# Optimization experiments

Measured on AMD Instinct MI355X. Metric: run time of the kernel, lower is better.

Reference implementation:

```python
import jax, jax.numpy as jnp
import numpy as np

# Multi-scale feature pyramid (static: determines per-level slice bounds)
SPATIAL_SHAPES = np.array([[100, 100], [50, 50], [25, 25], [13, 13], [7, 7]])  # (H, W) per level
LEVEL_START = np.concatenate([[0], np.cumsum(SPATIAL_SHAPES[:, 0] * SPATIAL_SHAPES[:, 1])])[:-1]
C = 256       # hidden_inplanes
HEADS = 8     # head_nums
POINTS = 4    # point_nums
LEVELS = 5    # feature_level_nums
FF = 2048     # feedforward_planes
DH = C // HEADS


def setup_inputs() -> dict:
    key = jax.random.key(0)
    ks = jax.random.split(key, 16)
    B = 2
    L = int((SPATIAL_SHAPES[:, 0] * SPATIAL_SHAPES[:, 1]).sum())  # 13343 tokens
    s = 0.02
    return {
        'src': jax.random.normal(ks[0], (B, L, C), jnp.float32),
        'pos': jax.random.normal(ks[1], (B, L, C), jnp.float32) * 0.1,
        'reference_points': jax.random.uniform(ks[2], (B, L, LEVELS, 2), jnp.float32),
        'wv': jax.random.normal(ks[3], (C, C), jnp.float32) * s,
        'bv': jnp.zeros((C,), jnp.float32),
        'wo': jax.random.normal(ks[4], (C, HEADS * LEVELS * POINTS * 2), jnp.float32) * s,
        'bo': jax.random.normal(ks[5], (HEADS * LEVELS * POINTS * 2,), jnp.float32) * 0.5,
        'wa': jax.random.normal(ks[6], (C, HEADS * LEVELS * POINTS), jnp.float32) * s,
        'ba': jnp.zeros((HEADS * LEVELS * POINTS,), jnp.float32),
        'wout': jax.random.normal(ks[7], (C, C), jnp.float32) * s,
        'bout': jnp.zeros((C,), jnp.float32),
        'ln1g': jnp.ones((C,), jnp.float32),
        'ln1b': jnp.zeros((C,), jnp.float32),
        'w1': jax.random.normal(ks[8], (C, FF), jnp.float32) * s,
        'b1': jnp.zeros((FF,), jnp.float32),
        'w2': jax.random.normal(ks[9], (FF, C), jnp.float32) * s,
        'b2': jnp.zeros((C,), jnp.float32),
        'ln2g': jnp.ones((C,), jnp.float32),
        'ln2b': jnp.zeros((C,), jnp.float32),
    }


def layernorm(x, g, b, eps=1e-5):
    m = jnp.mean(x, -1, keepdims=True)
    v = jnp.var(x, -1, keepdims=True)
    return (x - m) * jax.lax.rsqrt(v + eps) * g + b


def bilinear_sample(val, loc, Hs, Ws):
    # val: [B, heads, H*W, dh]   loc: [B, heads, Lq, P, 2] normalized coords in [0,1]
    # grid_sample semantics, align_corners=False, zero padding outside
    px = loc[..., 0] * Ws - 0.5
    py = loc[..., 1] * Hs - 0.5
    x0 = jnp.floor(px); y0 = jnp.floor(py)
    lx = px - x0;       ly = py - y0
    x0i = x0.astype(jnp.int32); y0i = y0.astype(jnp.int32)
    gather = jax.vmap(jax.vmap(lambda v, i: v[i]))  # over batch, head dims
    out = jnp.zeros(loc.shape[:-1] + (val.shape[-1],), val.dtype)
    for dx, dy, w in ((0, 0, (1 - lx) * (1 - ly)), (1, 0, lx * (1 - ly)),
                      (0, 1, (1 - lx) * ly), (1, 1, lx * ly)):
        xi = x0i + dx; yi = y0i + dy
        valid = (xi >= 0) & (xi < Ws) & (yi >= 0) & (yi < Hs)
        idx = jnp.clip(yi, 0, Hs - 1) * Ws + jnp.clip(xi, 0, Ws - 1)
        g = gather(val, idx)  # [B, heads, Lq, P, dh]
        out = out + (w * valid)[..., None] * g
    return out


def msdeform_attn(query, value_in, ref, wv, bv, wo, bo, wa, ba, wout, bout):
    B, Lq, _ = query.shape
    # value projection -> [B, heads, Len, dh]
    value = (value_in @ wv + bv).reshape(B, -1, HEADS, DH).transpose(0, 2, 1, 3)
    offsets = (query @ wo + bo).reshape(B, Lq, HEADS, LEVELS, POINTS, 2)
    attn = jax.nn.softmax((query @ wa + ba).reshape(B, Lq, HEADS, LEVELS * POINTS), -1)
    attn = attn.reshape(B, Lq, HEADS, LEVELS, POINTS)
    # offset normalizer = (W, H) per level
    norml = jnp.asarray(SPATIAL_SHAPES[:, ::-1].copy(), jnp.float32)
    loc = ref[:, :, None, :, None, :] + offsets / norml[None, None, None, :, None, :]
    acc = jnp.zeros((B, Lq, HEADS, DH), query.dtype)
    for l in range(LEVELS):
        Hs, Ws = int(SPATIAL_SHAPES[l, 0]), int(SPATIAL_SHAPES[l, 1])
        s = int(LEVEL_START[l])
        vl = value[:, :, s:s + Hs * Ws, :]
        locl = jnp.transpose(loc[:, :, :, l], (0, 2, 1, 3, 4))  # [B, heads, Lq, P, 2]
        samp = bilinear_sample(vl, locl, Hs, Ws)                 # [B, heads, Lq, P, dh]
        acc = acc + jnp.einsum('bhqpd,bqhp->bqhd', samp, attn[:, :, :, l])
    return acc.reshape(B, Lq, C) @ wout + bout


def reference(src, pos, reference_points, wv, bv, wo, bo, wa, ba, wout, bout,
              ln1g, ln1b, w1, b1, w2, b2, ln2g, ln2b):
    # DeformableTransformerEncoderLayer (eval mode, dropout off)
    q = src + pos
    src2 = msdeform_attn(q, src, reference_points, wv, bv, wo, bo, wa, ba, wout, bout)
    x = layernorm(src + src2, ln1g, ln1b)
    ffn = jax.nn.relu(x @ w1 + b1) @ w2 + b2
    return layernorm(x + ffn, ln2g, ln2b)
```

## Files before the change

### kernel.cpp

```cpp
#include <hip/hip_runtime.h>
#include <hip/hip_bf16.h>
#include <hip/hip_fp16.h>

typedef __hip_bfloat16 bf16;
typedef unsigned short ushort_t;
typedef __attribute__((ext_vector_type(8))) short bf16x8;
typedef __attribute__((ext_vector_type(16))) float f32x16;

__device__ __forceinline__ float us2f(unsigned short u) {
    unsigned int x = ((unsigned int)u) << 16;
    return __uint_as_float(x);
}
__device__ __forceinline__ ushort_t f2us(float f) {
    return ((__hip_bfloat16_raw)__float2bfloat16(f)).x;
}

__device__ __forceinline__ void gl_lds16(const ushort_t* g, ushort_t* l) {
    __builtin_amdgcn_global_load_lds(
        (const __attribute__((address_space(1))) void*)g,
        (__attribute__((address_space(3))) void*)l, 16, 0, 0);
}

__global__ __launch_bounds__(256) void cast2_kernel(
    const float* __restrict__ src, const float* __restrict__ pos,
    bf16* __restrict__ src_b, bf16* __restrict__ q_b, int n)
{
    int i = (blockIdx.x * 256 + threadIdx.x) * 4;
    if (i < n) {
        const float4 s4 = *reinterpret_cast<const float4*>(&src[i]);
        const float4 p4 = *reinterpret_cast<const float4*>(&pos[i]);
        int2 sp, qp;
        sp.x = (unsigned)f2us(s4.x) | ((unsigned)f2us(s4.y) << 16);
        sp.y = (unsigned)f2us(s4.z) | ((unsigned)f2us(s4.w) << 16);
        qp.x = (unsigned)f2us(s4.x + p4.x) | ((unsigned)f2us(s4.y + p4.y) << 16);
        qp.y = (unsigned)f2us(s4.z + p4.z) | ((unsigned)f2us(s4.w + p4.w) << 16);
        *reinterpret_cast<int2*>((ushort_t*)src_b + i) = sp;
        *reinterpret_cast<int2*>((ushort_t*)q_b + i) = qp;
    }
}

__global__ __launch_bounds__(256) void prep_kernel(
    const float* __restrict__ wv, const float* __restrict__ wo,
    const float* __restrict__ wa, const float* __restrict__ wout,
    const float* __restrict__ w1, const float* __restrict__ w2,
    const float* __restrict__ bo, const float* __restrict__ ba,
    bf16* __restrict__ wvt, bf16* __restrict__ wcat,
    ushort_t* __restrict__ woutp,
    ushort_t* __restrict__ w1p, ushort_t* __restrict__ w2p,
    float* __restrict__ bcat)
{
    __shared__ float tile[32][33];
    const int b = blockIdx.x;
    const float* W; bf16* Wt = nullptr; ushort_t* Wp = nullptr;
    int K, N, tb, mode = 0;
    if (b < 64)        { W = wv;   Wt = wvt;            K = 256;  N = 256;  tb = b; }
    else if (b < 144)  { W = wo;   Wt = wcat;           K = 256;  N = 320;  tb = b - 64; }
    else if (b < 184)  { W = wa;   Wt = wcat + 320*256; K = 256;  N = 160;  tb = b - 144; }
    else if (b < 248)  { W = wout; Wp = woutp; mode = 1; K = 256; N = 256;  tb = b - 184; }
    else if (b < 760)  { W = w1;   Wp = w1p; mode = 1;  K = 256;  N = 2048; tb = b - 248; }
    else if (b < 1272) { W = w2;   Wp = w2p; mode = 2;  K = 2048; N = 256;  tb = b - 760; }
    else {
        int i = (b - 1272) * 256 + threadIdx.x;
        if (i < 320) bcat[i] = bo[i];
        else if (i < 480) bcat[i] = ba[i - 320];
        return;
    }
    const int ntn = N >> 5;
    const int nb = (tb % ntn) * 32, kb = (tb / ntn) * 32;
    const int tx = threadIdx.x & 31, ty = threadIdx.x >> 5;
    #pragma unroll
    for (int i = 0; i < 32; i += 8) {
        int k = kb + ty + i, n = nb + tx;
        tile[ty + i][tx] = (k < K && n < N) ? W[(size_t)k * N + n] : 0.f;
    }
    __syncthreads();
    if (mode == 0) {
        #pragma unroll
        for (int i = 0; i < 32; i += 8) {
            int n = nb + ty + i, k = kb + tx;
            if (n < N && k < K)
                Wt[(size_t)n * K + k] = __float2bfloat16(tile[tx][ty + i]);
        }
    } else if (threadIdx.x < 128) {
        const int l = threadIdx.x & 63, kw = threadIdx.x >> 6;
        const int kb8 = kw * 16 + (l >> 5) * 8;
        const int nx = l & 31;
        ushort_t tmp[8];
        #pragma unroll
        for (int e = 0; e < 8; ++e) tmp[e] = f2us(tile[kb8 + e][nx]);
        size_t base;
        if (mode == 1)
            base = ((size_t)(((nb >> 5) * 8 + (kb >> 5)) * 2 + kw)) * 512;
        else
            base = ((size_t)((((kb >> 7) * 8 + (nb >> 5)) * 4 + ((kb >> 5) & 3)) * 2 + kw)) * 512;
        *reinterpret_cast<int4*>(Wp + base + l * 8) =
            *reinterpret_cast<const int4*>(tmp);
    }
}

template<bool RELU, bool OUT_BF16, bool HAS_RESID, bool RESID_BF16, int NT, int WPE>
__global__ __launch_bounds__(256, WPE) void gemm_mfma_s(
    const ushort_t* __restrict__ A,
    const ushort_t* __restrict__ Bt,
    const float* __restrict__ bias,
    const void* __restrict__ residv,
    void* __restrict__ outv, int M, int N, int K, int mtiles)
{
    __shared__ __align__(16) char smemraw[24576];
    ushort_t* Asmem = (ushort_t*)smemraw;
    ushort_t* Bsmem = (ushort_t*)(smemraw + 4096);
    float (*epi)[68] = (float(*)[68])smemraw;

    const int lid = blockIdx.x;
    const int tbk = lid >> 3;
    const int xb = tbk & (NT - 1);
    const int yg = (tbk / NT) * 8 + (lid & 7);
    if (yg >= mtiles) return;
    const int m0 = yg * 64;
    const int n0 = xb * 128;

    const int tid = threadIdx.x;
    const int lane = tid & 63;
    const int wave = tid >> 6;
    const int l32 = lane & 31;
    const int hi  = lane >> 5;
    const int wm = wave >> 1;
    const int wn = wave & 1;

    const int lsup = lane >> 3;
    const int clin = lane & 7;

    const int gsA = wave * 8 + lsup;
    const int csA = clin ^ (gsA & 7);
    int rA = m0 + gsA * 2 + (csA >> 2); if (rA > M - 1) rA = M - 1;
    const ushort_t* aP = A + (size_t)rA * K + (csA & 3) * 8;
    ushort_t* aL = Asmem + wave * 512;

    const ushort_t* bP[2]; ushort_t* bL[2];
    #pragma unroll
    for (int i = 0; i < 2; ++i) {
        const int gsB = wave * 16 + i * 8 + lsup;
        const int csB = clin ^ (gsB & 7);
        int rB = n0 + gsB * 2 + (csB >> 2); if (rB > N - 1) rB = N - 1;
        bP[i] = Bt + (size_t)rB * K + (csB & 3) * 8;
        bL[i] = Bsmem + (wave * 16 + i * 8) * 64;
    }

    const int arow = wm * 32 + l32;
    const int asup = arow >> 1;
    const ushort_t* aR[2];
    #pragma unroll
    for (int kw = 0; kw < 2; ++kw) {
        const int q = kw * 2 + hi;
        const int slot = (((arow & 1) << 2) | q) ^ (asup & 7);
        aR[kw] = Asmem + asup * 64 + slot * 8;
    }
    const ushort_t* bR[2][2];
    #pragma unroll
    for (int j = 0; j < 2; ++j) {
        const int brow = wn * 64 + j * 32 + l32;
        const int bsup = brow >> 1;
        #pragma unroll
        for (int kw = 0; kw < 2; ++kw) {
            const int q = kw * 2 + hi;
            const int slot = (((brow & 1) << 2) | q) ^ (bsup & 7);
            bR[j][kw] = Bsmem + bsup * 64 + slot * 8;
        }
    }

    f32x16 acc[2] = {};

    auto stage = [&](int ofs) {
        gl_lds16(aP, aL + ofs);             aP    += 32;
        gl_lds16(bP[0], bL[0] + ofs);       bP[0] += 32;
        gl_lds16(bP[1], bL[1] + ofs);       bP[1] += 32;
    };
    auto compute = [&](int ofs) {
        #pragma unroll
        for (int kw = 0; kw < 2; ++kw) {
            const bf16x8 af = *reinterpret_cast<const bf16x8*>(aR[kw] + ofs);
            #pragma unroll
            for (int j = 0; j < 2; ++j)
                acc[j] = __builtin_amdgcn_mfma_f32_32x32x16_bf16(
                    af, *reinterpret_cast<const bf16x8*>(bR[j][kw] + ofs),
                    acc[j], 0, 0, 0);
        }
    };

    const int ntile = K >> 5;
    stage(0);
    for (int t = 0; t < ntile; t += 2) {
        __syncthreads();
        stage(6144);
        compute(0);
        __syncthreads();
        if (t + 2 < ntile) stage(0);
        compute(6144);
    }
    __syncthreads();

    #pragma unroll
    for (int half = 0; half < 2; ++half) {
        if (wn == half) {
            #pragma unroll
            for (int j = 0; j < 2; ++j) {
                const int coll = j * 32 + l32;
                const int n = n0 + half * 64 + coll;
                const float bv = (n < N) ? bias[n] : 0.f;
                #pragma unroll
                for (int r = 0; r < 16; ++r) {
                    const int row = wm * 32 + hi * 4 + (r & 3) + (r >> 2) * 8;
                    epi[row][coll] = acc[j][r] + bv;
                }
            }
        }
        __syncthreads();
        #pragma unroll
        for (int i = 0; i < 4; ++i) {
            const int idx = i * 256 + tid;
            const int row = idx >> 4;
            const int c4  = idx & 15;
            const int m = m0 + row;
            const int n = n0 + half * 64 + c4 * 4;
            if (m < M && n + 3 < N) {
                float4 v = *reinterpret_cast<const float4*>(&epi[row][c4 * 4]);
                if (HAS_RESID) {
                    if (RESID_BF16) {
                        const int2 rw = *reinterpret_cast<const int2*>(
                            (const ushort_t*)residv + (size_t)m * N + n);
                        v.x += us2f((ushort_t)((unsigned)rw.x & 0xffffu));
                        v.y += us2f((ushort_t)((unsigned)rw.x >> 16));
                        v.z += us2f((ushort_t)((unsigned)rw.y & 0xffffu));
                        v.w += us2f((ushort_t)((unsigned)rw.y >> 16));
                    } else {
                        const float4 r4 = *reinterpret_cast<const float4*>(
                            (const float*)residv + (size_t)m * N + n);
                        v.x += r4.x; v.y += r4.y; v.z += r4.z; v.w += r4.w;
                    }
                }
                if (RELU) {
                    v.x = fmaxf(v.x, 0.f); v.y = fmaxf(v.y, 0.f);
                    v.z = fmaxf(v.z, 0.f); v.w = fmaxf(v.w, 0.f);
                }
                if (OUT_BF16) {
                    int2 pk;
                    pk.x = (unsigned)f2us(v.x) | ((unsigned)f2us(v.y) << 16);
                    pk.y = (unsigned)f2us(v.z) | ((unsigned)f2us(v.w) << 16);
                    *reinterpret_cast<int2*>((ushort_t*)outv + (size_t)m * N + n) = pk;
                } else {
                    *reinterpret_cast<float4*>((float*)outv + (size_t)m * N + n) = v;
                }
            }
        }
        if (half == 0) __syncthreads();
    }
}

template<bool RELU, bool OUT_BF16, bool HAS_RESID, bool RESID_BF16, int NT>
__global__ __launch_bounds__(256, 4) void gemm_mfma_b(
    const ushort_t* __restrict__ A,
    const ushort_t* __restrict__ Bt,
    const float* __restrict__ bias,
    const void* __restrict__ residv,
    void* __restrict__ outv, int M, int N, int K, int mtiles)
{
    __shared__ __align__(16) char smemraw[32768];
    ushort_t* Asmem = (ushort_t*)smemraw;
    ushort_t* Bsmem = (ushort_t*)(smemraw + 8192);
    float (*epi)[68] = (float(*)[68])smemraw;

    const int lid = blockIdx.x;
    const int tbk = lid >> 3;
    const int xb = tbk & (NT - 1);
    const int yg = (tbk / NT) * 8 + (lid & 7);
    if (yg >= mtiles) return;
    const int m0 = yg * 128;
    const int n0 = xb * 128;

    const int tid = threadIdx.x;
    const int lane = tid & 63;
    const int wave = tid >> 6;
    const int l32 = lane & 31;
    const int hi  = lane >> 5;
    const int wm = wave >> 1;
    const int wn = wave & 1;

    const int lsup = lane >> 3;
    const int clin = lane & 7;
    const ushort_t *aP[2], *bP[2];
    ushort_t *aL[2], *bL[2];
    #pragma unroll
    for (int i = 0; i < 2; ++i) {
        const int gs = wave * 16 + i * 8 + lsup;
        const int cs = clin ^ (gs & 7);
        int rA = m0 + gs * 2 + (cs >> 2); if (rA > M - 1) rA = M - 1;
        aP[i] = A + (size_t)rA * K + (cs & 3) * 8;
        aL[i] = Asmem + (wave * 16 + i * 8) * 64;
        int rB = n0 + gs * 2 + (cs >> 2); if (rB > N - 1) rB = N - 1;
        bP[i] = Bt + (size_t)rB * K + (cs & 3) * 8;
        bL[i] = Bsmem + (wave * 16 + i * 8) * 64;
    }

    const ushort_t* aR[2][2];
    const ushort_t* bR[2][2];
    #pragma unroll
    for (int mi = 0; mi < 2; ++mi) {
        const int arow = wm * 64 + mi * 32 + l32;
        const int asup = arow >> 1;
        #pragma unroll
        for (int kw = 0; kw < 2; ++kw) {
            const int q = kw * 2 + hi;
            const int slot = (((arow & 1) << 2) | q) ^ (asup & 7);
            aR[mi][kw] = Asmem + asup * 64 + slot * 8;
        }
    }
    #pragma unroll
    for (int ni = 0; ni < 2; ++ni) {
        const int brow = wn * 64 + ni * 32 + l32;
        const int bsup = brow >> 1;
        #pragma unroll
        for (int kw = 0; kw < 2; ++kw) {
            const int q = kw * 2 + hi;
            const int slot = (((brow & 1) << 2) | q) ^ (bsup & 7);
            bR[ni][kw] = Bsmem + bsup * 64 + slot * 8;
        }
    }

    f32x16 a00 = {}, a01 = {}, a10 = {}, a11 = {};

    auto stage = [&](int ofs) {
        gl_lds16(aP[0], aL[0] + ofs); aP[0] += 32;
        gl_lds16(aP[1], aL[1] + ofs); aP[1] += 32;
        gl_lds16(bP[0], bL[0] + ofs); bP[0] += 32;
        gl_lds16(bP[1], bL[1] + ofs); bP[1] += 32;
    };
    auto compute = [&](int ofs) {
        #pragma unroll
        for (int kw = 0; kw < 2; ++kw) {
            const bf16x8 af0 = *reinterpret_cast<const bf16x8*>(aR[0][kw] + ofs);
            const bf16x8 af1 = *reinterpret_cast<const bf16x8*>(aR[1][kw] + ofs);
            const bf16x8 bf0 = *reinterpret_cast<const bf16x8*>(bR[0][kw] + ofs);
            const bf16x8 bf1 = *reinterpret_cast<const bf16x8*>(bR[1][kw] + ofs);
            a00 = __builtin_amdgcn_mfma_f32_32x32x16_bf16(af0, bf0, a00, 0, 0, 0);
            a01 = __builtin_amdgcn_mfma_f32_32x32x16_bf16(af0, bf1, a01, 0, 0, 0);
            a10 = __builtin_amdgcn_mfma_f32_32x32x16_bf16(af1, bf0, a10, 0, 0, 0);
            a11 = __builtin_amdgcn_mfma_f32_32x32x16_bf16(af1, bf1, a11, 0, 0, 0);
        }
    };

    const int ntile = K >> 5;
    stage(0);
    for (int t = 0; t < ntile; t += 2) {
        __syncthreads();
        stage(8192);
        compute(0);
        __syncthreads();
        if (t + 2 < ntile) stage(0);
        compute(8192);
    }
    __syncthreads();

    #pragma unroll
    for (int qd = 0; qd < 4; ++qd) {
        const int rh = qd >> 1, ch = qd & 1;
        if (qd) __syncthreads();
        if (wm == rh && wn == ch) {
            #pragma unroll
            for (int ni = 0; ni < 2; ++ni) {
                const int col = ni * 32 + l32;
                const int n = n0 + ch * 64 + col;
                const float bv = (n < N) ? bias[n] : 0.f;
                #pragma unroll
                for (int mi = 0; mi < 2; ++mi) {
                    const f32x16& ac = (mi == 0) ? (ni == 0 ? a00 : a01)
                                                 : (ni == 0 ? a10 : a11);
                    #pragma unroll
                    for (int r = 0; r < 16; ++r) {
                        const int row = mi * 32 + hi * 4 + (r & 3) + (r >> 2) * 8;
                        epi[row][col] = ac[r] + bv;
                    }
                }
            }
        }
        __syncthreads();
        #pragma unroll
        for (int i = 0; i < 4; ++i) {
            const int idx = i * 256 + tid;
            const int row = idx >> 4;
            const int c4  = idx & 15;
            const int m = m0 + rh * 64 + row;
            const int n = n0 + ch * 64 + c4 * 4;
            if (m < M && n + 3 < N) {
                float4 v = *reinterpret_cast<const float4*>(&epi[row][c4 * 4]);
                if (HAS_RESID) {
                    if (RESID_BF16) {
                        const int2 rw = *reinterpret_cast<const int2*>(
                            (const ushort_t*)residv + (size_t)m * N + n);
                        v.x += us2f((ushort_t)((unsigned)rw.x & 0xffffu));
                        v.y += us2f((ushort_t)((unsigned)rw.x >> 16));
                        v.z += us2f((ushort_t)((unsigned)rw.y & 0xffffu));
                        v.w += us2f((ushort_t)((unsigned)rw.y >> 16));
                    } else {
                        const float4 r4 = *reinterpret_cast<const float4*>(
                            (const float*)residv + (size_t)m * N + n);
                        v.x += r4.x; v.y += r4.y; v.z += r4.z; v.w += r4.w;
                    }
                }
                if (RELU) {
                    v.x = fmaxf(v.x, 0.f); v.y = fmaxf(v.y, 0.f);
                    v.z = fmaxf(v.z, 0.f); v.w = fmaxf(v.w, 0.f);
                }
                if (OUT_BF16) {
                    int2 pk;
                    pk.x = (unsigned)f2us(v.x) | ((unsigned)f2us(v.y) << 16);
                    pk.y = (unsigned)f2us(v.z) | ((unsigned)f2us(v.w) << 16);
                    *reinterpret_cast<int2*>((ushort_t*)outv + (size_t)m * N + n) = pk;
                } else {
                    *reinterpret_cast<float4*>((float*)outv + (size_t)m * N + n) = v;
                }
            }
        }
    }
}

__global__ __launch_bounds__(256, 4) void woutln_kernel(
    const ushort_t* __restrict__ A,
    const ushort_t* __restrict__ Wp,
    const float* __restrict__ bias,
    const float* __restrict__ resid,
    const float* __restrict__ g, const float* __restrict__ beta,
    bf16* __restrict__ out, int M)
{
    __shared__ __align__(16) char smem[33280];
    ushort_t* Xs = (ushort_t*)smem;
    float (*epi)[260] = (float(*)[260])smem;

    const int m0 = blockIdx.x * 32;
    const int tid = threadIdx.x;
    const int lane = tid & 63;
    const int wave = tid >> 6;
    const int l32 = lane & 31;
    const int hi  = lane >> 5;

    {
        const int lsup = (wave & 1) * 8 + (lane >> 3);
        const int clin = lane & 7;
        const int cs = clin ^ (lsup & 7);
        int r = m0 + lsup * 2 + (cs >> 2); if (r > M - 1) r = M - 1;
        const ushort_t* xp = A + (size_t)r * 256 + (cs & 3) * 8;
        ushort_t* xl = Xs + (wave & 1) * 512;
        #pragma unroll
        for (int p = 0; p < 4; ++p) {
            const int t = p * 2 + (wave >> 1);
            gl_lds16(xp + t * 32, xl + t * 1024);
        }
    }

    int aOff[2];
    {
        const int sr = l32 >> 1;
        #pragma unroll
        for (int kw = 0; kw < 2; ++kw) {
            const int q = kw * 2 + hi;
            const int slot = (((l32 & 1) << 2) | q) ^ (sr & 7);
            aOff[kw] = sr * 64 + slot * 8;
        }
    }

    f32x16 za0 = {}, za1 = {};
    __syncthreads();

    const int nq0 = wave * 2;
    #pragma unroll
    for (int t = 0; t < 8; ++t) {
        #pragma unroll
        for (int kw = 0; kw < 2; ++kw) {
            const bf16x8 af = *reinterpret_cast<const bf16x8*>(
                Xs + t * 1024 + aOff[kw]);
            const bf16x8 b0 = *reinterpret_cast<const bf16x8*>(
                Wp + ((nq0 * 8 + t) * 2 + kw) * 512 + lane * 8);
            const bf16x8 b1 = *reinterpret_cast<const bf16x8*>(
                Wp + (((nq0 + 1) * 8 + t) * 2 + kw) * 512 + lane * 8);
            za0 = __builtin_amdgcn_mfma_f32_32x32x16_bf16(af, b0, za0, 0, 0, 0);
            za1 = __builtin_amdgcn_mfma_f32_32x32x16_bf16(af, b1, za1, 0, 0, 0);
        }
    }

    __syncthreads();

    #pragma unroll
    for (int j = 0; j < 2; ++j) {
        const int col = wave * 64 + j * 32 + l32;
        const float bz = bias[col];
        const f32x16& zz = j ? za1 : za0;
        #pragma unroll
        for (int r = 0; r < 16; ++r)
            epi[(r & 3) + 8 * (r >> 2) + 4 * hi][col] = zz[r] + bz;
    }
    __syncthreads();

    const int row = tid >> 3, t8 = tid & 7;
    const int m = m0 + row;
    const int mc = (m < M) ? m : (M - 1);
    const float* xr = resid + (size_t)mc * 256 + t8 * 32;
    float v[32];
    float s = 0.f, ss = 0.f;
    #pragma unroll
    for (int i = 0; i < 8; ++i) {
        const float4 e = *reinterpret_cast<const float4*>(
            &epi[row][t8 * 32 + i * 4]);
        const float4 r4 = *reinterpret_cast<const float4*>(xr + i * 4);
        const float f0 = e.x + r4.x;
        const float f1 = e.y + r4.y;
        const float f2 = e.z + r4.z;
        const float f3 = e.w + r4.w;
        v[i * 4]     = f0; v[i * 4 + 1] = f1;
        v[i * 4 + 2] = f2; v[i * 4 + 3] = f3;
        s  += f0 + f1 + f2 + f3;
        ss += f0 * f0 + f1 * f1 + f2 * f2 + f3 * f3;
    }
    s += __shfl_xor(s, 1); ss += __shfl_xor(ss, 1);
    s += __shfl_xor(s, 2); ss += __shfl_xor(ss, 2);
    s += __shfl_xor(s, 4); ss += __shfl_xor(ss, 4);
    const float mean = s * (1.f / 256.f);
    const float var = ss * (1.f / 256.f) - mean * mean;
    const float rs = rsqrtf(var + 1e-5f);
    if (m < M) {
        #pragma unroll
        for (int i = 0; i < 8; ++i) {
            const float4 g4 = *reinterpret_cast<const float4*>(
                &g[t8 * 32 + i * 4]);
            const float4 b4 = *reinterpret_cast<const float4*>(
                &beta[t8 * 32 + i * 4]);
            float4 o4;
            o4.x = (v[i * 4]     - mean) * rs * g4.x + b4.x;
            o4.y = (v[i * 4 + 1] - mean) * rs * g4.y + b4.y;
            o4.z = (v[i * 4 + 2] - mean) * rs * g4.z + b4.z;
            o4.w = (v[i * 4 + 3] - mean) * rs * g4.w + b4.w;
            int2 pk;
            pk.x = (unsigned)f2us(o4.x) | ((unsigned)f2us(o4.y) << 16);
            pk.y = (unsigned)f2us(o4.z) | ((unsigned)f2us(o4.w) << 16);
            *reinterpret_cast<int2*>(
                (ushort_t*)out + (size_t)m * 256 + t8 * 32 + i * 4) = pk;
        }
    }
}

__global__ __launch_bounds__(256, 3) void ffn_fused2(
    const ushort_t* __restrict__ X,
    const ushort_t* __restrict__ W1p,
    const ushort_t* __restrict__ W2p,
    const float* __restrict__ b1, const float* __restrict__ b2,
    const float* __restrict__ g, const float* __restrict__ beta,
    float* __restrict__ out, int M)
{
    __shared__ __align__(16) char smem[33280];
    ushort_t* Xs = (ushort_t*)smem;
    ushort_t* Hs = (ushort_t*)(smem + 16384);
    float (*epi)[260] = (float(*)[260])smem;

    const int m0 = blockIdx.x * 32;
    const int tid = threadIdx.x;
    const int lane = tid & 63;
    const int wave = tid >> 6;
    const int l32 = lane & 31;
    const int hi  = lane >> 5;

    {
        const int lsup = (wave & 1) * 8 + (lane >> 3);
        const int clin = lane & 7;
        const int cs = clin ^ (lsup & 7);
        int r = m0 + lsup * 2 + (cs >> 2); if (r > M - 1) r = M - 1;
        const ushort_t* xp = X + (size_t)r * 256 + (cs & 3) * 8;
        ushort_t* xl = Xs + (wave & 1) * 512;
        #pragma unroll
        for (int p = 0; p < 4; ++p) {
            const int t = p * 2 + (wave >> 1);
            gl_lds16(xp + t * 32, xl + t * 1024);
        }
    }

    int aOff[2];
    {
        const int sr = l32 >> 1;
        #pragma unroll
        for (int kw = 0; kw < 2; ++kw) {
            const int q = kw * 2 + hi;
            const int slot = (((l32 & 1) << 2) | q) ^ (sr & 7);
            aOff[kw] = sr * 64 + slot * 8;
        }
    }
    int hadr[16];
    #pragma unroll
    for (int r = 0; r < 16; ++r) {
        const int m = (r & 3) + 8 * (r >> 2) + 4 * hi;
        const int slot = (((m & 1) << 2) | (l32 >> 3)) ^ ((m >> 1) & 7);
        hadr[r] = wave * 1024 + (m >> 1) * 64 + slot * 8 + (l32 & 7);
    }

    f32x16 za0 = {}, za1 = {};
    __syncthreads();

    for (int c = 0; c < 16; ++c) {
        f32x16 h0 = {}, h1 = {};
        const int hcg = c * 4 + wave;
        const ushort_t* w1c = W1p + (size_t)hcg * 8192;
        #pragma unroll
        for (int t = 0; t < 8; t += 2) {
            #pragma unroll
            for (int kw = 0; kw < 2; ++kw) {
                const bf16x8 a0 = *reinterpret_cast<const bf16x8*>(
                    Xs + t * 1024 + aOff[kw]);
                const bf16x8 a1 = *reinterpret_cast<const bf16x8*>(
                    Xs + (t + 1) * 1024 + aOff[kw]);
                const bf16x8 b0 = *reinterpret_cast<const bf16x8*>(
                    w1c + (t * 2 + kw) * 512 + lane * 8);
                const bf16x8 b1f = *reinterpret_cast<const bf16x8*>(
                    w1c + ((t + 1) * 2 + kw) * 512 + lane * 8);
                h0 = __builtin_amdgcn_mfma_f32_32x32x16_bf16(a0, b0, h0, 0, 0, 0);
                h1 = __builtin_amdgcn_mfma_f32_32x32x16_bf16(a1, b1f, h1, 0, 0, 0);
            }
        }
        const float bb = b1[hcg * 32 + l32];

        __syncthreads();
        #pragma unroll
        for (int r = 0; r < 16; ++r)
            Hs[hadr[r]] = f2us(fmaxf(h0[r] + h1[r] + bb, 0.f));
        __syncthreads();

        const ushort_t* w2c = W2p + (size_t)c * 32768;
        const int nq0 = wave * 2;
        #pragma unroll
        for (int t = 0; t < 4; ++t) {
            #pragma unroll
            for (int kw = 0; kw < 2; ++kw) {
                const bf16x8 af = *reinterpret_cast<const bf16x8*>(
                    Hs + t * 1024 + aOff[kw]);
                const bf16x8 bf0 = *reinterpret_cast<const bf16x8*>(
                    w2c + ((nq0 * 4 + t) * 2 + kw) * 512 + lane * 8);
                const bf16x8 bf1 = *reinterpret_cast<const bf16x8*>(
                    w2c + (((nq0 + 1) * 4 + t) * 2 + kw) * 512 + lane * 8);
                za0 = __builtin_amdgcn_mfma_f32_32x32x16_bf16(af, bf0, za0, 0, 0, 0);
                za1 = __builtin_amdgcn_mfma_f32_32x32x16_bf16(af, bf1, za1, 0, 0, 0);
            }
        }
    }

    __syncthreads();

    #pragma unroll
    for (int j = 0; j < 2; ++j) {
        const int col = wave * 64 + j * 32 + l32;
        const float bz = b2[col];
        const f32x16& zz = j ? za1 : za0;
        #pragma unroll
        for (int r = 0; r < 16; ++r)
            epi[(r & 3) + 8 * (r >> 2) + 4 * hi][col] = zz[r] + bz;
    }
    __syncthreads();

    const int row = tid >> 3, t8 = tid & 7;
    const int m = m0 + row;
    const int mc = (m < M) ? m : (M - 1);
    const ushort_t* xr = X + (size_t)mc * 256 + t8 * 32;
    float v[32];
    float s = 0.f, ss = 0.f;
    #pragma unroll
    for (int i = 0; i < 8; ++i) {
        const float4 e = *reinterpret_cast<const float4*>(
            &epi[row][t8 * 32 + i * 4]);
        const int2 rb = *reinterpret_cast<const int2*>(xr + i * 4);
        const float f0 = e.x + us2f((ushort_t)((unsigned)rb.x & 0xffffu));
        const float f1 = e.y + us2f((ushort_t)((unsigned)rb.x >> 16));
        const float f2 = e.z + us2f((ushort_t)((unsigned)rb.y & 0xffffu));
        const float f3 = e.w + us2f((ushort_t)((unsigned)rb.y >> 16));
        v[i * 4]     = f0; v[i * 4 + 1] = f1;
        v[i * 4 + 2] = f2; v[i * 4 + 3] = f3;
        s  += f0 + f1 + f2 + f3;
        ss += f0 * f0 + f1 * f1 + f2 * f2 + f3 * f3;
    }
    s += __shfl_xor(s, 1); ss += __shfl_xor(ss, 1);
    s += __shfl_xor(s, 2); ss += __shfl_xor(ss, 2);
    s += __shfl_xor(s, 4); ss += __shfl_xor(ss, 4);
    const float mean = s * (1.f / 256.f);
    const float var = ss * (1.f / 256.f) - mean * mean;
    const float rs = rsqrtf(var + 1e-5f);
    if (m < M) {
        #pragma unroll
        for (int i = 0; i < 8; ++i) {
            const float4 g4 = *reinterpret_cast<const float4*>(
                &g[t8 * 32 + i * 4]);
            const float4 b4 = *reinterpret_cast<const float4*>(
                &beta[t8 * 32 + i * 4]);
            float4 o4;
            o4.x = (v[i * 4]     - mean) * rs * g4.x + b4.x;
            o4.y = (v[i * 4 + 1] - mean) * rs * g4.y + b4.y;
            o4.z = (v[i * 4 + 2] - mean) * rs * g4.z + b4.z;
            o4.w = (v[i * 4 + 3] - mean) * rs * g4.w + b4.w;
            *reinterpret_cast<float4*>(
                &out[(size_t)m * 256 + t8 * 32 + i * 4]) = o4;
        }
    }
}

__global__ __launch_bounds__(256) void msda_kernel_v7(
    const ushort_t* __restrict__ og,
    const float* __restrict__ refp,
    const ushort_t* __restrict__ value,
    bf16* __restrict__ out,
    int M, int L)
{
    const int tid = threadIdx.x;
    const int nb = gridDim.x;
    int wk = blockIdx.x;
    if ((nb & 7) == 0) {
        const int per = nb >> 3;
        wk = (blockIdx.x & 7) * per + (blockIdx.x >> 3);
    }
    const int qbase = wk * 8;

    __shared__ float s_attn[8][160];
    __shared__ int2  s_off[1280];
    __shared__ int2  s_wh[1280];

    for (int i = tid; i < 1280; i += 256) {
        int q = i / 160, j = i - q * 160;
        int qq = qbase + q;
        s_attn[q][j] = (qq < M) ? us2f(og[(size_t)qq * 480 + 320 + j]) : 0.f;
    }
    __syncthreads();

    if (tid < 64) {
        float* a = &s_attn[tid >> 3][(tid & 7) * 20];
        float mx = -1e30f;
        #pragma unroll
        for (int i = 0; i < 20; ++i) mx = fmaxf(mx, a[i]);
        float ssum = 0.f;
        #pragma unroll
        for (int i = 0; i < 20; ++i) {
            float e = __expf(a[i] - mx);
            a[i] = e;
            ssum += e;
        }
        float inv = 1.f / ssum;
        #pragma unroll
        for (int i = 0; i < 20; ++i) a[i] *= inv;
    }
    __syncthreads();

    #pragma unroll
    for (int it = 0; it < 5; ++it) {
        const int t = tid + it * 256;
        const int q  = t / 160;
        const int r  = t - q * 160;
        const int l  = (r - (r / 20) * 20) >> 2;
        const int qq = qbase + q;

        int2 offp = {0, 0};
        __half2 h01 = __floats2half2_rn(0.f, 0.f);
        __half2 h23 = h01;
        if (qq < M) {
            const int Wi = (l == 0) ? 100 : (l == 1) ? 50 : (l == 2) ? 25
                         : (l == 3) ? 13 : 7;
            const int s0 = (l == 0) ? 0 : (l == 1) ? 10000 : (l == 2) ? 12500
                         : (l == 3) ? 13125 : 13294;
            const float Wf = (float)Wi;
            const float ox = us2f(og[(size_t)qq * 480 + r * 2]);
            const float oy = us2f(og[(size_t)qq * 480 + r * 2 + 1]);
            const float2 rf = *reinterpret_cast<const float2*>(
                &refp[(size_t)qq * 10 + l * 2]);
            const float a = s_attn[q][r];

            const float px = fmaf(rf.x, Wf, -0.5f) + ox;
            const float py = fmaf(rf.y, Wf, -0.5f) + oy;
            const float x0f = floorf(px);
            const float y0f = floorf(py);
            const float lx = px - x0f;
            const float ly = py - y0f;
            const int x0 = (int)x0f;
            const int y0 = (int)y0f;

            const float wx0v = (x0 >= 0 && x0 < Wi) ? (1.f - lx) : 0.f;
            const float wx1v = (x0 + 1 >= 0 && x0 + 1 < Wi) ? lx : 0.f;
            const float wy0v = (y0 >= 0 && y0 < Wi) ? (1.f - ly) : 0.f;
            const float wy1v = (y0 + 1 >= 0 && y0 + 1 < Wi) ? ly : 0.f;

            const int c0 = min(max(x0, 0), Wi - 2);
            const int r0 = min(max(y0, 0), Wi - 2);
            const float swx0 = (x0 == c0 ? wx0v : 0.f) + (x0 + 1 == c0 ? wx1v : 0.f);
            const float swx1 = (x0 == c0 + 1 ? wx0v : 0.f) + (x0 + 1 == c0 + 1 ? wx1v : 0.f);
            const float swy0 = (y0 == r0 ? wy0v : 0.f) + (y0 + 1 == r0 ? wy1v : 0.f);
            const float swy1 = (y0 == r0 + 1 ? wy0v : 0.f) + (y0 + 1 == r0 + 1 ? wy1v : 0.f);

            offp.x = (s0 + r0 * Wi + c0) * 512;
            offp.y = offp.x + Wi * 512;
            h01 = __floats2half2_rn(a * swx0 * swy0, a * swx1 * swy0);
            h23 = __floats2half2_rn(a * swx0 * swy1, a * swx1 * swy1);
        }
        s_off[t] = offp;
        union { __half2 h; int i; } c0u, c1u;
        c0u.h = h01; c1u.h = h23;
        int2 wpk; wpk.x = c0u.i; wpk.y = c1u.i;
        s_wh[t] = wpk;
    }
    __syncthreads();

    const int qi  = tid >> 5;
    const int g   = tid & 31;
    const int h   = g >> 2;
    const int sub = g & 3;
    const int bq = qbase + qi;
    if (bq >= M) return;
    const int b = bq / L;

    const char* vb = (const char*)value + (size_t)b * L * 512 + h * 64 + sub * 16;

    float acc[8] = {};
    const int tb = qi * 160 + h * 20;
    #pragma unroll 2
    for (int p = 0; p < 20; ++p) {
        const int2 off = s_off[tb + p];
        const int2 whp = s_wh[tb + p];
        const int4 u00 = *reinterpret_cast<const int4*>(vb + off.x);
        const int4 u10 = *reinterpret_cast<const int4*>(vb + off.x + 512);
        const int4 u01 = *reinterpret_cast<const int4*>(vb + off.y);
        const int4 u11 = *reinterpret_cast<const int4*>(vb + off.y + 512);
        union { int i; __half2 h; } w0u, w1u;
        w0u.i = whp.x; w1u.i = whp.y;
        const float2 w01 = __half22float2(w0u.h);
        const float2 w23 = __half22float2(w1u.h);
        #define ACC4(u, wt)                                                        \
            acc[0] = fmaf(wt, __uint_as_float((unsigned)(u).x << 16), acc[0]);      \
            acc[1] = fmaf(wt, __uint_as_float((unsigned)(u).x & 0xffff0000u), acc[1]); \
            acc[2] = fmaf(wt, __uint_as_float((unsigned)(u).y << 16), acc[2]);      \
            acc[3] = fmaf(wt, __uint_as_float((unsigned)(u).y & 0xffff0000u), acc[3]); \
            acc[4] = fmaf(wt, __uint_as_float((unsigned)(u).z << 16), acc[4]);      \
            acc[5] = fmaf(wt, __uint_as_float((unsigned)(u).z & 0xffff0000u), acc[5]); \
            acc[6] = fmaf(wt, __uint_as_float((unsigned)(u).w << 16), acc[6]);      \
            acc[7] = fmaf(wt, __uint_as_float((unsigned)(u).w & 0xffff0000u), acc[7]);
        ACC4(u00, w01.x)
        ACC4(u10, w01.y)
        ACC4(u01, w23.x)
        ACC4(u11, w23.y)
        #undef ACC4
    }

    ushort_t o[8];
    #pragma unroll
    for (int i = 0; i < 8; ++i) o[i] = f2us(acc[i]);
    int4 pkt;
    pkt.x = (int)o[0] | ((int)o[1] << 16);
    pkt.y = (int)o[2] | ((int)o[3] << 16);
    pkt.z = (int)o[4] | ((int)o[5] << 16);
    pkt.w = (int)o[6] | ((int)o[7] << 16);
    *reinterpret_cast<int4*>((ushort_t*)out + (size_t)bq * 256 + h * 32 + sub * 8) = pkt;
}

extern "C" void kernel_launch(void* const* d_in, const int* in_sizes, int n_in,
                              void* d_out, int out_size, void* d_ws, size_t ws_size,
                              hipStream_t stream)
{
    const int B = 2, L = 13343, C = 256;
    const int M = B * L;

    const float* src  = (const float*)d_in[0];
    const float* pos  = (const float*)d_in[1];
    const float* refp = (const float*)d_in[2];
    const float* wv   = (const float*)d_in[3];
    const float* bv   = (const float*)d_in[4];
    const float* wo   = (const float*)d_in[5];
    const float* bo   = (const float*)d_in[6];
    const float* wa   = (const float*)d_in[7];
    const float* ba   = (const float*)d_in[8];
    const float* wout = (const float*)d_in[9];
    const float* bout = (const float*)d_in[10];
    const float* ln1g = (const float*)d_in[11];
    const float* ln1b = (const float*)d_in[12];
    const float* w1   = (const float*)d_in[13];
    const float* b1   = (const float*)d_in[14];
    const float* w2   = (const float*)d_in[15];
    const float* b2   = (const float*)d_in[16];
    const float* ln2g = (const float*)d_in[17];
    const float* ln2b = (const float*)d_in[18];

    char* ws = (char*)d_ws;
    const size_t MB = 1ull << 20;
    bf16*  src_b  = (bf16*)(ws + 0);
    bf16*  q_b    = (bf16*)(ws + 14 * MB);
    bf16*  val_b  = (bf16*)(ws + 28 * MB);
    bf16*  og     = (bf16*)(ws + 42 * MB);
    bf16*  acc_b  = (bf16*)(ws + 95 * MB);
    bf16*  x_b    = (bf16*)(ws + 138 * MB);
    bf16* wvt    = (bf16*)(ws + 152 * MB);
    bf16* wcat   = wvt + 256 * 256;
    ushort_t* woutp = (ushort_t*)(wcat + 480 * 256);
    ushort_t* w1p = woutp + 256 * 256;
    ushort_t* w2p = w1p + 2048 * 256;
    float* bcat  = (float*)(w2p + 256 * 2048);
    (void)ws_size; (void)n_in; (void)in_sizes; (void)out_size;

    const int mt64  = (M + 63) / 64;
    const int gm8   = (mt64 + 7) / 8;
    const int mt128 = (M + 127) / 128;
    const int gb8   = (mt128 + 7) / 8;
    const int mt32  = (M + 31) / 32;

    prep_kernel<<<1274, 256, 0, stream>>>(wv, wo, wa, wout, w1, w2, bo, ba,
                                          wvt, wcat, woutp, w1p, w2p, bcat);

    cast2_kernel<<<(M * C / 4 + 255) / 256, 256, 0, stream>>>(
        src, pos, src_b, q_b, M * C);

    gemm_mfma_s<false, true, false, false, 2, 4><<<gm8 * 16, 256, 0, stream>>>(
        (const ushort_t*)src_b, (const ushort_t*)wvt, bv, nullptr, val_b,
        M, 256, 256, mt64);

    gemm_mfma_b<false, true, false, false, 4><<<gb8 * 32, 256, 0, stream>>>(
        (const ushort_t*)q_b, (const ushort_t*)wcat, bcat, nullptr, og,
        M, 480, 256, mt128);

    msda_kernel_v7<<<(M + 7) / 8, 256, 0, stream>>>(
        (const ushort_t*)og, refp, (const ushort_t*)val_b, acc_b, M, L);

    woutln_kernel<<<mt32, 256, 0, stream>>>(
        (const ushort_t*)acc_b, woutp, bout, src, ln1g, ln1b, x_b, M);

    ffn_fused2<<<mt32, 256, 0, stream>>>(
        (const ushort_t*)x_b, w1p, w2p, b1, b2, ln2g, ln2b,
        (float*)d_out, M);
}
```

Measured before the change: 355.5 us.

## Double FFN row tile to 64 so each weight fragment feeds two MFMA tiles

The fused FFN kernel now processes 64 rows per block instead of 32. Each W1/W2 fragment loaded from global memory is reused for two row halves, which halves weight traffic per row and raises the ratio of MFMA work to loads. In exchange, LDS per block grows to 48KB, there are twice as many accumulator registers, and launch bounds drop to 2 blocks per CU. The grid is also halved, so fewer blocks are available to cover latency.

```diff
diff --git a/kernel.cpp b/kernel.cpp
--- a/kernel.cpp
+++ b/kernel.cpp
@@ -546,7 +546,7 @@
     }
 }
 
-__global__ __launch_bounds__(256, 3) void ffn_fused2(
+__global__ __launch_bounds__(256, 2) void ffn_fused5(
     const ushort_t* __restrict__ X,
     const ushort_t* __restrict__ W1p,
     const ushort_t* __restrict__ W2p,
@@ -554,25 +554,26 @@
     const float* __restrict__ g, const float* __restrict__ beta,
     float* __restrict__ out, int M)
 {
-    __shared__ __align__(16) char smem[33280];
+    __shared__ __align__(16) char smem[49152];
     ushort_t* Xs = (ushort_t*)smem;
-    ushort_t* Hs = (ushort_t*)(smem + 16384);
+    ushort_t* Hs = (ushort_t*)(smem + 32768);
     float (*epi)[260] = (float(*)[260])smem;
 
-    const int m0 = blockIdx.x * 32;
+    const int m0 = blockIdx.x * 64;
     const int tid = threadIdx.x;
     const int lane = tid & 63;
     const int wave = tid >> 6;
     const int l32 = lane & 31;
     const int hi  = lane >> 5;
 
-    {
+    #pragma unroll
+    for (int hf = 0; hf < 2; ++hf) {
         const int lsup = (wave & 1) * 8 + (lane >> 3);
         const int clin = lane & 7;
         const int cs = clin ^ (lsup & 7);
-        int r = m0 + lsup * 2 + (cs >> 2); if (r > M - 1) r = M - 1;
+        int r = m0 + hf * 32 + lsup * 2 + (cs >> 2); if (r > M - 1) r = M - 1;
         const ushort_t* xp = X + (size_t)r * 256 + (cs & 3) * 8;
-        ushort_t* xl = Xs + (wave & 1) * 512;
+        ushort_t* xl = Xs + hf * 8192 + (wave & 1) * 512;
         #pragma unroll
         for (int p = 0; p < 4; ++p) {
             const int t = p * 2 + (wave >> 1);
@@ -598,35 +599,43 @@
         hadr[r] = wave * 1024 + (m >> 1) * 64 + slot * 8 + (l32 & 7);
     }
 
-    f32x16 za0 = {}, za1 = {};
+    f32x16 za00 = {}, za01 = {}, za10 = {}, za11 = {};
     __syncthreads();
 
     for (int c = 0; c < 16; ++c) {
-        f32x16 h0 = {}, h1 = {};
+        f32x16 h0a = {}, h1a = {}, h0b = {}, h1b = {};
         const int hcg = c * 4 + wave;
         const ushort_t* w1c = W1p + (size_t)hcg * 8192;
         #pragma unroll
         for (int t = 0; t < 8; t += 2) {
             #pragma unroll
             for (int kw = 0; kw < 2; ++kw) {
-                const bf16x8 a0 = *reinterpret_cast<const bf16x8*>(
-                    Xs + t * 1024 + aOff[kw]);
-                const bf16x8 a1 = *reinterpret_cast<const bf16x8*>(
-                    Xs + (t + 1) * 1024 + aOff[kw]);
                 const bf16x8 b0 = *reinterpret_cast<const bf16x8*>(
                     w1c + (t * 2 + kw) * 512 + lane * 8);
                 const bf16x8 b1f = *reinterpret_cast<const bf16x8*>(
                     w1c + ((t + 1) * 2 + kw) * 512 + lane * 8);
-                h0 = __builtin_amdgcn_mfma_f32_32x32x16_bf16(a0, b0, h0, 0, 0, 0);
-                h1 = __builtin_amdgcn_mfma_f32_32x32x16_bf16(a1, b1f, h1, 0, 0, 0);
+                const bf16x8 a0a = *reinterpret_cast<const bf16x8*>(
+                    Xs + t * 1024 + aOff[kw]);
+                const bf16x8 a1a = *reinterpret_cast<const bf16x8*>(
+                    Xs + (t + 1) * 1024 + aOff[kw]);
+                const bf16x8 a0b = *reinterpret_cast<const bf16x8*>(
+                    Xs + 8192 + t * 1024 + aOff[kw]);
+                const bf16x8 a1b = *reinterpret_cast<const bf16x8*>(
+                    Xs + 8192 + (t + 1) * 1024 + aOff[kw]);
+                h0a = __builtin_amdgcn_mfma_f32_32x32x16_bf16(a0a, b0, h0a, 0, 0, 0);
+                h1a = __builtin_amdgcn_mfma_f32_32x32x16_bf16(a1a, b1f, h1a, 0, 0, 0);
+                h0b = __builtin_amdgcn_mfma_f32_32x32x16_bf16(a0b, b0, h0b, 0, 0, 0);
+                h1b = __builtin_amdgcn_mfma_f32_32x32x16_bf16(a1b, b1f, h1b, 0, 0, 0);
             }
         }
         const float bb = b1[hcg * 32 + l32];
 
         __syncthreads();
         #pragma unroll
-        for (int r = 0; r < 16; ++r)
-            Hs[hadr[r]] = f2us(fmaxf(h0[r] + h1[r] + bb, 0.f));
+        for (int r = 0; r < 16; ++r) {
+            Hs[hadr[r]]        = f2us(fmaxf(h0a[r] + h1a[r] + bb, 0.f));
+            Hs[4096 + hadr[r]] = f2us(fmaxf(h0b[r] + h1b[r] + bb, 0.f));
+        }
         __syncthreads();
 
         const ushort_t* w2c = W2p + (size_t)c * 32768;
@@ -635,14 +644,18 @@
         for (int t = 0; t < 4; ++t) {
             #pragma unroll
             for (int kw = 0; kw < 2; ++kw) {
-                const bf16x8 af = *reinterpret_cast<const bf16x8*>(
-                    Hs + t * 1024 + aOff[kw]);
                 const bf16x8 bf0 = *reinterpret_cast<const bf16x8*>(
                     w2c + ((nq0 * 4 + t) * 2 + kw) * 512 + lane * 8);
                 const bf16x8 bf1 = *reinterpret_cast<const bf16x8*>(
                     w2c + (((nq0 + 1) * 4 + t) * 2 + kw) * 512 + lane * 8);
-                za0 = __builtin_amdgcn_mfma_f32_32x32x16_bf16(af, bf0, za0, 0, 0, 0);
-                za1 = __builtin_amdgcn_mfma_f32_32x32x16_bf16(af, bf1, za1, 0, 0, 0);
+                const bf16x8 afa = *reinterpret_cast<const bf16x8*>(
+                    Hs + t * 1024 + aOff[kw]);
+                const bf16x8 afb = *reinterpret_cast<const bf16x8*>(
+                    Hs + 4096 + t * 1024 + aOff[kw]);
+                za00 = __builtin_amdgcn_mfma_f32_32x32x16_bf16(afa, bf0, za00, 0, 0, 0);
+                za01 = __builtin_amdgcn_mfma_f32_32x32x16_bf16(afa, bf1, za01, 0, 0, 0);
+                za10 = __builtin_amdgcn_mfma_f32_32x32x16_bf16(afb, bf0, za10, 0, 0, 0);
+                za11 = __builtin_amdgcn_mfma_f32_32x32x16_bf16(afb, bf1, za11, 0, 0, 0);
             }
         }
     }
@@ -650,56 +663,61 @@
     __syncthreads();
 
     #pragma unroll
-    for (int j = 0; j < 2; ++j) {
-        const int col = wave * 64 + j * 32 + l32;
-        const float bz = b2[col];
-        const f32x16& zz = j ? za1 : za0;
-        #pragma unroll
-        for (int r = 0; r < 16; ++r)
-            epi[(r & 3) + 8 * (r >> 2) + 4 * hi][col] = zz[r] + bz;
-    }
-    __syncthreads();
-
-    const int row = tid >> 3, t8 = tid & 7;
-    const int m = m0 + row;
-    const int mc = (m < M) ? m : (M - 1);
-    const ushort_t* xr = X + (size_t)mc * 256 + t8 * 32;
-    float v[32];
-    float s = 0.f, ss = 0.f;
-    #pragma unroll
-    for (int i = 0; i < 8; ++i) {
-        const float4 e = *reinterpret_cast<const float4*>(
-            &epi[row][t8 * 32 + i * 4]);
-        const int2 rb = *reinterpret_cast<const int2*>(xr + i * 4);
-        const float f0 = e.x + us2f((ushort_t)((unsigned)rb.x & 0xffffu));
-        const float f1 = e.y + us2f((ushort_t)((unsigned)rb.x >> 16));
-        const float f2 = e.z + us2f((ushort_t)((unsigned)rb.y & 0xffffu));
-        const float f3 = e.w + us2f((ushort_t)((unsigned)rb.y >> 16));
-        v[i * 4]     = f0; v[i * 4 + 1] = f1;
-        v[i * 4 + 2] = f2; v[i * 4 + 3] = f3;
-        s  += f0 + f1 + f2 + f3;
-        ss += f0 * f0 + f1 * f1 + f2 * f2 + f3 * f3;
-    }
-    s += __shfl_xor(s, 1); ss += __shfl_xor(ss, 1);
-    s += __shfl_xor(s, 2); ss += __shfl_xor(ss, 2);
-    s += __shfl_xor(s, 4); ss += __shfl_xor(ss, 4);
-    const float mean = s * (1.f / 256.f);
-    const float var = ss * (1.f / 256.f) - mean * mean;
-    const float rs = rsqrtf(var + 1e-5f);
-    if (m < M) {
+    for (int p = 0; p < 2; ++p) {
+        if (p) __syncthreads();
+        #pragma unroll
+        for (int j = 0; j < 2; ++j) {
+            const int col = wave * 64 + j * 32 + l32;
+            const float bz = b2[col];
+            const f32x16& zz = (p == 0) ? (j ? za01 : za00)
+                                        : (j ? za11 : za10);
+            #pragma unroll
+            for (int r = 0; r < 16; ++r)
+                epi[(r & 3) + 8 * (r >> 2) + 4 * hi][col] = zz[r] + bz;
+        }
+        __syncthreads();
+
+        const int row = tid >> 3, t8 = tid & 7;
+        const int m = m0 + p * 32 + row;
+        const int mc = (m < M) ? m : (M - 1);
+        const ushort_t* xr = X + (size_t)mc * 256 + t8 * 32;
+        float v[32];
+        float s = 0.f, ss = 0.f;
         #pragma unroll
         for (int i = 0; i < 8; ++i) {
-            const float4 g4 = *reinterpret_cast<const float4*>(
-                &g[t8 * 32 + i * 4]);
-            const float4 b4 = *reinterpret_cast<const float4*>(
-                &beta[t8 * 32 + i * 4]);
-            float4 o4;
-            o4.x = (v[i * 4]     - mean) * rs * g4.x + b4.x;
-            o4.y = (v[i * 4 + 1] - mean) * rs * g4.y + b4.y;
-            o4.z = (v[i * 4 + 2] - mean) * rs * g4.z + b4.z;
-            o4.w = (v[i * 4 + 3] - mean) * rs * g4.w + b4.w;
-            *reinterpret_cast<float4*>(
-                &out[(size_t)m * 256 + t8 * 32 + i * 4]) = o4;
+            const float4 e = *reinterpret_cast<const float4*>(
+                &epi[row][t8 * 32 + i * 4]);
+            const int2 rb = *reinterpret_cast<const int2*>(xr + i * 4);
+            const float f0 = e.x + us2f((ushort_t)((unsigned)rb.x & 0xffffu));
+            const float f1 = e.y + us2f((ushort_t)((unsigned)rb.x >> 16));
+            const float f2 = e.z + us2f((ushort_t)((unsigned)rb.y & 0xffffu));
+            const float f3 = e.w + us2f((ushort_t)((unsigned)rb.y >> 16));
+            v[i * 4]     = f0; v[i * 4 + 1] = f1;
+            v[i * 4 + 2] = f2; v[i * 4 + 3] = f3;
+            s  += f0 + f1 + f2 + f3;
+            ss += f0 * f0 + f1 * f1 + f2 * f2 + f3 * f3;
+        }
+        s += __shfl_xor(s, 1); ss += __shfl_xor(ss, 1);
+        s += __shfl_xor(s, 2); ss += __shfl_xor(ss, 2);
+        s += __shfl_xor(s, 4); ss += __shfl_xor(ss, 4);
+        const float mean = s * (1.f / 256.f);
+        const float var = ss * (1.f / 256.f) - mean * mean;
+        const float rs = rsqrtf(var + 1e-5f);
+        if (m < M) {
+            #pragma unroll
+            for (int i = 0; i < 8; ++i) {
+                const float4 g4 = *reinterpret_cast<const float4*>(
+                    &g[t8 * 32 + i * 4]);
+                const float4 b4 = *reinterpret_cast<const float4*>(
+                    &beta[t8 * 32 + i * 4]);
+                float4 o4;
+                o4.x = (v[i * 4]     - mean) * rs * g4.x + b4.x;
+                o4.y = (v[i * 4 + 1] - mean) * rs * g4.y + b4.y;
+                o4.z = (v[i * 4 + 2] - mean) * rs * g4.z + b4.z;
+                o4.w = (v[i * 4 + 3] - mean) * rs * g4.w + b4.w;
+                *reinterpret_cast<float4*>(
+                    &out[(size_t)m * 256 + t8 * 32 + i * 4]) = o4;
+            }
         }
     }
 }
@@ -926,7 +944,7 @@
     woutln_kernel<<<mt32, 256, 0, stream>>>(
         (const ushort_t*)acc_b, woutp, bout, src, ln1g, ln1b, x_b, M);
 
-    ffn_fused2<<<mt32, 256, 0, stream>>>(
+    ffn_fused5<<<mt64, 256, 0, stream>>>(
         (const ushort_t*)x_b, w1p, w2p, b1, b2, ln2g, ln2b,
         (float*)d_out, M);
 }
```

Result: faster. 338.7 us (median of 2 runs) (-4.7%).
